# Kernel optimization log

Hardware: AMD Instinct MI355X
Metric: run time of the kernel (lower is better)

## Reference

```python
import jax, jax.numpy as jnp
import numpy as np

B, T, D, KQ, K, V, L = 4, 4096, 256, 32, 4, 8, 4
LN_EPS = 1e-5


def _layernorm(h, g, b):
    mu = h.mean(-1, keepdims=True)
    var = ((h - mu) ** 2).mean(-1, keepdims=True)
    return (h - mu) * jax.lax.rsqrt(var + LN_EPS) * g + b


def _forward(x, attention_mask, Wq, bq, Wk, bk, Wg, bg, W1f, b1f, W2f, b2f,
             ln_g, ln_b, Whh, b_ih, b_hh, Wp, bp, opW1, opb1, opW2, opb2, Wo, bo):
    # ---- DemandRouter ----
    q = x @ Wq + bq                      # [B,T,KQ]
    k = x @ Wk + bk                      # [B,T,KQ]
    sim = jnp.einsum('btk,bsk->bts', q, k) / jnp.sqrt(jnp.float32(KQ))  # [B,T,T]
    mask2 = attention_mask[:, None, :] * attention_mask[:, :, None]
    sim = jnp.where(mask2 == 0, jnp.float32(-1e9), sim)
    gates = jax.nn.sigmoid(x @ Wg + bg)[..., 0]   # [B,T]
    sim = sim * gates[:, :, None]
    _, idx = jax.lax.top_k(sim, K)                # [B,T,K]
    gathered = jax.vmap(lambda xb, ib: xb[ib])(x, idx)  # [B,T,K,D]
    routed_mean = gathered.mean(axis=2)           # [B,T,D]
    # ---- System1Block ----
    ffn = jax.nn.gelu(routed_mean @ W1f + b1f, approximate=False) @ W2f + b2f
    h = _layernorm(routed_mean + ffn, ln_g, ln_b)  # [B,T,D]
    # ---- ProgramGenerator (GRU over zero inputs, h0 = mean-pooled context) ----
    hs = h.mean(axis=1)                           # [B,D]
    outs = []
    for _ in range(L):
        gh = hs @ Whh.T + b_hh                    # [B,3D]
        r = jax.nn.sigmoid(b_ih[:D] + gh[:, :D])
        z = jax.nn.sigmoid(b_ih[D:2 * D] + gh[:, D:2 * D])
        n = jnp.tanh(b_ih[2 * D:] + r * gh[:, 2 * D:])
        hs = (1 - z) * n + z * hs
        outs.append(hs)
    rnn_out = jnp.stack(outs, axis=1)             # [B,L,D]
    program_logits = rnn_out @ Wp + bp            # [B,L,V]
    # ---- NeuralOpLibrary: op outputs are identical across L, so compute once
    # on [B,T,D] and average softmax weights over L (same math as expand+mean).
    op_hidden = jax.nn.relu(jnp.einsum('btd,vde->btve', h, opW1) + opb1)
    op_out = jnp.einsum('btve,ved->btvd', op_hidden, opW2) + opb2  # [B,T,V,D]
    w = jax.nn.softmax(program_logits, axis=-1).mean(axis=1)       # [B,V]
    fused = jnp.einsum('bv,btvd->btd', w, op_out)                   # [B,T,D]
    # ---- pool + output projection ----
    pooled = fused.max(axis=1)                    # [B,D]
    return pooled @ Wo + bo


def setup_inputs() -> dict:
    key = jax.random.key(0)
    ks = jax.random.split(key, 20)
    s = 0.02
    p = lambda i, shape: jax.random.normal(ks[i], shape, jnp.float32) * s
    return {
        'x': jax.random.normal(ks[0], (B, T, D), jnp.float32),
        'attention_mask': jnp.ones((B, T), jnp.float32),
        'Wq': p(1, (D, KQ)), 'bq': jnp.zeros((KQ,), jnp.float32),
        'Wk': p(2, (D, KQ)), 'bk': jnp.zeros((KQ,), jnp.float32),
        'Wg': p(3, (D, 1)), 'bg': jnp.zeros((1,), jnp.float32),
        'W1f': p(4, (D, 2 * D)), 'b1f': jnp.zeros((2 * D,), jnp.float32),
        'W2f': p(5, (2 * D, D)), 'b2f': jnp.zeros((D,), jnp.float32),
        'ln_g': jnp.ones((D,), jnp.float32), 'ln_b': jnp.zeros((D,), jnp.float32),
        'Whh': p(6, (3 * D, D)), 'b_ih': p(7, (3 * D,)), 'b_hh': p(8, (3 * D,)),
        'Wp': p(9, (D, V)), 'bp': jnp.zeros((V,), jnp.float32),
        'opW1': p(10, (V, D, D)), 'opb1': jnp.zeros((V, D), jnp.float32),
        'opW2': p(11, (V, D, D)), 'opb2': jnp.zeros((V, D), jnp.float32),
        'Wo': p(12, (D, D)), 'bo': jnp.zeros((D,), jnp.float32),
    }


def reference(x, attention_mask, Wq, bq, Wk, bk, Wg, bg, W1f, b1f, W2f, b2f,
              ln_g, ln_b, Whh, b_ih, b_hh, Wp, bp, opW1, opb1, opW2, opb2, Wo, bo):
    return _forward(x, attention_mask, Wq, bq, Wk, bk, Wg, bg, W1f, b1f, W2f, b2f,
                    ln_g, ln_b, Whh, b_ih, b_hh, Wp, bp, opW1, opb1, opW2, opb2, Wo, bo)
```

## Files before the change

### kernel.cpp

```cpp
#include <hip/hip_runtime.h>

#define BB 4
#define TT 4096
#define DD 256
#define KQ 32
#define TOPK 4
#define NV 8
#define NL 4
#define MROWS (BB*TT)
#define NSC 8
#define SSPAN 512
#define NCAND (NSC*16)

typedef __attribute__((ext_vector_type(8))) __bf16 bf16x8;
typedef __attribute__((ext_vector_type(4))) float  f32x4;

__device__ __forceinline__ unsigned short f2bf(float f) {
  union { float f; unsigned u; } un; un.f = f;
  unsigned r = un.u + 0x7fffu + ((un.u >> 16) & 1u);
  return (unsigned short)(r >> 16);
}
__device__ __forceinline__ float b2f(unsigned short s) {
  union { unsigned u; float f; } un; un.u = ((unsigned)s) << 16;
  return un.f;
}

__device__ __forceinline__ void ins4(float val, int s, float v[4], int id[4]) {
  if (val <= v[3]) return;
  v[3] = val; id[3] = s;
  #pragma unroll
  for (int j = 3; j > 0; --j) {
    if (v[j] > v[j-1]) {
      float tv = v[j]; v[j] = v[j-1]; v[j-1] = tv;
      int   ti = id[j]; id[j] = id[j-1]; id[j-1] = ti;
    }
  }
}

__global__ __launch_bounds__(256) void prep_weights(
    const float* __restrict__ W1f, const float* __restrict__ W2f,
    const float* __restrict__ opW1, const float* __restrict__ opW2,
    const float* __restrict__ Whh,
    unsigned short* __restrict__ W1ft, unsigned short* __restrict__ W2ft,
    unsigned short* __restrict__ opW1t, unsigned short* __restrict__ opW2t,
    unsigned int* __restrict__ Whhp) {
  int idx = blockIdx.x * 256 + threadIdx.x;
  if (idx < 131072) { int n = idx >> 8, d = idx & 255; W1ft[idx] = f2bf(W1f[d*512 + n]); return; }
  idx -= 131072;
  if (idx < 131072) { int n = idx >> 9, d = idx & 511; W2ft[idx] = f2bf(W2f[d*256 + n]); return; }
  idx -= 131072;
  if (idx < 524288) { int np = idx >> 8, d = idx & 255; int v = np >> 8, e = np & 255;
                      opW1t[idx] = f2bf(opW1[v*65536 + d*256 + e]); return; }
  idx -= 524288;
  if (idx < 524288) { int n = idx >> 11, kp = idx & 2047; int v = kp >> 8, k2 = kp & 255;
                      opW2t[idx] = f2bf(opW2[v*65536 + k2*256 + n]); return; }
  idx -= 524288;
  if (idx < 98304) {
    int dp = idx / 768, j = idx - dp*768;
    unsigned lo = f2bf(Whh[j*256 + 2*dp]);
    unsigned hi = f2bf(Whh[j*256 + 2*dp + 1]);
    Whhp[idx] = lo | (hi << 16);
  }
}

__global__ __launch_bounds__(256) void qk_proj(
    const float* __restrict__ x, const float* __restrict__ Wq, const float* __restrict__ bq,
    const float* __restrict__ Wk, const float* __restrict__ bk,
    float* __restrict__ q, float* __restrict__ kk,
    unsigned short* __restrict__ qbf, unsigned short* __restrict__ kbf) {
  __shared__ float xs[1024];
  int tid = threadIdx.x;
  *(float4*)&xs[tid*4] = *(const float4*)&x[(size_t)blockIdx.x*1024 + tid*4];
  __syncthreads();
  int row = blockIdx.x*4 + (tid >> 6);
  int j = tid & 63;
  int jj = j & 31;
  const float* W = (j < 32) ? Wq : Wk;
  const float* xr = &xs[(tid >> 6) * 256];
  float acc = 0.f;
  #pragma unroll 8
  for (int d = 0; d < 256; ++d) acc += xr[d] * W[d*32 + jj];
  acc += (j < 32) ? bq[jj] : bk[jj];
  float* out = (j < 32) ? q : kk;
  unsigned short* outb = (j < 32) ? qbf : kbf;
  out[(size_t)row*32 + jj] = acc;
  outb[(size_t)row*32 + jj] = f2bf(acc);
}

__global__ __launch_bounds__(256) void sim_scan(
    const unsigned short* __restrict__ qbf, const unsigned short* __restrict__ kbf,
    const float* __restrict__ mask, int* __restrict__ candi, float* __restrict__ candvv) {
  int b = blockIdx.z, sc = blockIdx.y;
  int q0 = blockIdx.x * 64;
  int tid = threadIdx.x;
  int w = tid >> 6, lane = tid & 63;
  int l15 = lane & 15, lhi = lane >> 4;

  __shared__ unsigned short kfr[SSPAN*32];
  __shared__ float ms[SSPAN];
  __shared__ int mflag;

  int qrow = q0 + w*16 + l15;
  bf16x8 qf = *(const bf16x8*)&qbf[((size_t)b*TT + qrow)*32 + lhi*8];
  float mrow = mask[b*TT + qrow];

  float vtop[4]; int itop[4];
  #pragma unroll
  for (int r = 0; r < 4; ++r) { vtop[r] = -__builtin_inff(); itop[r] = 0; }

  int s0 = sc * SSPAN;
  if (tid == 0) mflag = 0;
  __syncthreads();
  int anyzero = 0;
  #pragma unroll
  for (int rr = 0; rr < 2; ++rr) {
    int s = rr*256 + tid;
    const unsigned short* src = &kbf[((size_t)b*TT + s0 + s)*32];
    uint4 d0 = *(const uint4*)(src);
    uint4 d1 = *(const uint4*)(src + 8);
    uint4 d2 = *(const uint4*)(src + 16);
    uint4 d3 = *(const uint4*)(src + 24);
    int fb = (s >> 4)*512 + (s & 15)*8;
    *(uint4*)&kfr[fb +   0] = d0;
    *(uint4*)&kfr[fb + 128] = d1;
    *(uint4*)&kfr[fb + 256] = d2;
    *(uint4*)&kfr[fb + 384] = d3;
    float mv = mask[b*TT + s0 + s];
    ms[s] = mv;
    if (mv == 0.f) anyzero = 1;
  }
  if (anyzero) mflag = 1;
  __syncthreads();
  bool useMask = (mflag != 0) || (mrow == 0.f);
  f32x4 z = {0.f, 0.f, 0.f, 0.f};
  for (int sf = 0; sf < SSPAN/16; sf += 2) {
    bf16x8 a0 = *(const bf16x8*)&kfr[(sf+0)*512 + lane*8];
    bf16x8 a1 = *(const bf16x8*)&kfr[(sf+1)*512 + lane*8];
    f32x4 c0 = __builtin_amdgcn_mfma_f32_16x16x32_bf16(a0, qf, z, 0, 0, 0);
    f32x4 c1 = __builtin_amdgcn_mfma_f32_16x16x32_bf16(a1, qf, z, 0, 0, 0);
    int sb0 = s0 + (sf+0)*16 + lhi*4;
    int sb1 = s0 + (sf+1)*16 + lhi*4;
    #pragma unroll
    for (int r = 0; r < 4; ++r) {
      float v0 = c0[r], v1 = c1[r];
      if (useMask) {
        if (mrow * ms[(sf+0)*16 + lhi*4 + r] == 0.f) v0 = -1e9f;
        if (mrow * ms[(sf+1)*16 + lhi*4 + r] == 0.f) v1 = -1e9f;
      }
      ins4(v0, sb0 + r, vtop, itop);
      ins4(v1, sb1 + r, vtop, itop);
    }
  }
  size_t base = ((size_t)(b*TT + qrow))*NCAND + sc*16 + lhi*4;
  #pragma unroll
  for (int r = 0; r < 4; ++r) { candi[base + r] = itop[r]; candvv[base + r] = vtop[r]; }
}

__global__ __launch_bounds__(256) void refine8(
    const int* __restrict__ candi, const float* __restrict__ candv,
    const float* __restrict__ q, const float* __restrict__ kk,
    const float* __restrict__ mask, int* __restrict__ sel) {
  int tid = threadIdx.x;
  int g = tid >> 5, j = tid & 31;
  int row = blockIdx.x*8 + g;
  int b = row >> 12;
  float v[4]; int id[4];
  const float* cvp = &candv[(size_t)row*NCAND];
  const int*   cip = &candi[(size_t)row*NCAND];
  #pragma unroll
  for (int k2 = 0; k2 < 4; ++k2) { v[k2] = cvp[j + k2*32]; id[k2] = cip[j + k2*32]; }
  int c8[8];
  #pragma unroll
  for (int r = 0; r < 8; ++r) {
    float bv = v[0]; int bi = id[0];
    #pragma unroll
    for (int k2 = 1; k2 < 4; ++k2)
      if (v[k2] > bv || (v[k2] == bv && id[k2] < bi)) { bv = v[k2]; bi = id[k2]; }
    #pragma unroll
    for (int o = 16; o > 0; o >>= 1) {
      float ov = __shfl_xor(bv, o, 32);
      int   oi = __shfl_xor(bi, o, 32);
      if (ov > bv || (ov == bv && oi < bi)) { bv = ov; bi = oi; }
    }
    c8[r] = bi;
    #pragma unroll
    for (int k2 = 0; k2 < 4; ++k2) if (id[k2] == bi) v[k2] = -__builtin_inff();
  }
  int ca = c8[j >> 2];
  int seg = (j & 3) * 8;
  const float* kp = &kk[((size_t)(b << 12) + ca)*32 + seg];
  const float* qp = &q[(size_t)row*32 + seg];
  float pd = 0.f;
  #pragma unroll
  for (int t = 0; t < 8; t += 4) {
    float4 kv = *(const float4*)&kp[t];
    float4 qv = *(const float4*)&qp[t];
    pd += kv.x*qv.x + kv.y*qv.y + kv.z*qv.z + kv.w*qv.w;
  }
  pd += __shfl_xor(pd, 1, 32);
  pd += __shfl_xor(pd, 2, 32);
  if (mask[row] * mask[(b << 12) + ca] == 0.f) pd = -1e9f;
  float dv[8];
  #pragma unroll
  for (int c = 0; c < 8; ++c) dv[c] = __shfl(pd, c*4, 32);
  if (j == 0) {
    int s0 = -1, s1 = -1, s2 = -1, s3 = -1;
    int4 o4;
    #pragma unroll
    for (int r = 0; r < 4; ++r) {
      float bv = -__builtin_inff(); int bi = 0x7fffffff;
      #pragma unroll
      for (int c = 0; c < 8; ++c) {
        int ii = c8[c]; float vv = dv[c];
        if (ii == s0 || ii == s1 || ii == s2 || ii == s3) continue;
        if (vv > bv || (vv == bv && ii < bi)) { bv = vv; bi = ii; }
      }
      if (r == 0) { o4.x = bi; s0 = bi; }
      else if (r == 1) { o4.y = bi; s1 = bi; }
      else if (r == 2) { o4.z = bi; s2 = bi; }
      else { o4.w = bi; s3 = bi; }
    }
    *(int4*)&sel[(size_t)row*4] = o4;
  }
}

__global__ __launch_bounds__(256) void gather_mean(
    const int* __restrict__ sel, const float* __restrict__ x,
    unsigned short* __restrict__ rmb) {
  int tid = threadIdx.x;
  int row = blockIdx.x*4 + (tid >> 6);
  int lane = tid & 63;
  int b = row >> 12;
  int4 s = *(const int4*)&sel[(size_t)row*4];
  const float* xb = &x[(size_t)b*TT*DD];
  float4 a  = *(const float4*)&xb[(size_t)s.x*DD + lane*4];
  float4 bb = *(const float4*)&xb[(size_t)s.y*DD + lane*4];
  float4 cc = *(const float4*)&xb[(size_t)s.z*DD + lane*4];
  float4 e  = *(const float4*)&xb[(size_t)s.w*DD + lane*4];
  ushort4 o;
  o.x = f2bf((a.x + bb.x + cc.x + e.x)*0.25f);
  o.y = f2bf((a.y + bb.y + cc.y + e.y)*0.25f);
  o.z = f2bf((a.z + bb.z + cc.z + e.z)*0.25f);
  o.w = f2bf((a.w + bb.w + cc.w + e.w)*0.25f);
  *(ushort4*)&rmb[(size_t)row*DD + lane*4] = o;
}

template<int EPI>
__global__ __launch_bounds__(256) void gemm_bf16(
    const unsigned short* __restrict__ A, const unsigned short* __restrict__ Bt,
    int Ndim, int Kdim,
    const float* __restrict__ bias,
    const unsigned short* __restrict__ resB,
    const float* __restrict__ auxf,
    float* __restrict__ outF, unsigned short* __restrict__ outB) {
  __shared__ unsigned short SMEM[128*132];
  unsigned short* As = SMEM;
  unsigned short* Bs = SMEM + 128*64;
  int tid = threadIdx.x;
  int lane = tid & 63, wid = tid >> 6;
  int wm = wid >> 1, wn = wid & 1;
  int l16 = lane & 15, lhi = lane >> 4;
  int m0 = blockIdx.x * 128, n0 = blockIdx.y * 128;
  f32x4 acc[4][4] = {};
  for (int kt = 0; kt < Kdim; kt += 64) {
    __syncthreads();
    #pragma unroll
    for (int i = 0; i < 4; ++i) {
      int L = i*256 + tid;
      int r = L >> 3, c = L & 7;
      int cs = c ^ (r & 7);
      uint4 va = *(const uint4*)(A  + (size_t)(m0 + r)*Kdim + kt + c*8);
      *(uint4*)&As[r*64 + cs*8] = va;
      uint4 vb = *(const uint4*)(Bt + (size_t)(n0 + r)*Kdim + kt + c*8);
      *(uint4*)&Bs[r*64 + cs*8] = vb;
    }
    __syncthreads();
    #pragma unroll
    for (int ks = 0; ks < 2; ++ks) {
      bf16x8 af[4], bfr[4];
      int kc = ks*4 + lhi;
      #pragma unroll
      for (int f = 0; f < 4; ++f) {
        int ra = wm*64 + f*16 + l16;
        af[f]  = *(const bf16x8*)&As[ra*64 + ((kc ^ (ra & 7)))*8];
        int rb = wn*64 + f*16 + l16;
        bfr[f] = *(const bf16x8*)&Bs[rb*64 + ((kc ^ (rb & 7)))*8];
      }
      #pragma unroll
      for (int mf = 0; mf < 4; ++mf)
        #pragma unroll
        for (int nf = 0; nf < 4; ++nf)
          acc[mf][nf] = __builtin_amdgcn_mfma_f32_16x16x32_bf16(af[mf], bfr[nf], acc[mf][nf], 0, 0, 0);
    }
  }
  if constexpr (EPI == 1) {
    #pragma unroll
    for (int mf = 0; mf < 4; ++mf)
      #pragma unroll
      for (int nf = 0; nf < 4; ++nf)
        #pragma unroll
        for (int r = 0; r < 4; ++r) {
          int row = m0 + wm*64 + mf*16 + lhi*4 + r;
          int col = n0 + wn*64 + nf*16 + l16;
          float v = acc[mf][nf][r] + bias[col] + b2f(resB[(size_t)row*Ndim + col]);
          outF[(size_t)row*Ndim + col] = v;
        }
  } else {
    __syncthreads();
    #pragma unroll
    for (int mf = 0; mf < 4; ++mf) {
      #pragma unroll
      for (int nf = 0; nf < 4; ++nf) {
        #pragma unroll
        for (int r = 0; r < 4; ++r) {
          int lrow = wm*64 + mf*16 + lhi*4 + r;
          int lcol = wn*64 + nf*16 + l16;
          int row = m0 + lrow, col = n0 + lcol;
          float v = acc[mf][nf][r];
          if constexpr (EPI == 0) {
            v += bias[col];
            v = 0.5f * v * (1.0f + erff(v * 0.70710678118654752f));
          } else if constexpr (EPI == 2) {
            v += bias[col];
            v = fmaxf(v, 0.0f) * auxf[(row >> 12)*8 + (col >> 8)];
          } else {
            v += auxf[(row >> 12)*256 + col];
          }
          SMEM[lrow*132 + lcol] = f2bf(v);
        }
      }
    }
    __syncthreads();
    #pragma unroll
    for (int i = 0; i < 8; ++i) {
      int idx = i*256 + tid;
      int lrow = idx >> 4, co = (idx & 15)*8;
      *(uint4*)&outB[(size_t)(m0 + lrow)*Ndim + n0 + co] = *(const uint4*)&SMEM[lrow*132 + co];
    }
  }
}

__global__ __launch_bounds__(256) void gemm64_bf16(
    const unsigned short* __restrict__ A, const unsigned short* __restrict__ Bt,
    int Ndim, int Kdim,
    const float* __restrict__ auxf, unsigned short* __restrict__ outB) {
  __shared__ unsigned short SMEM[64*192 + 64];
  unsigned short* As = SMEM;
  unsigned short* Bs = SMEM + 64*64;
  int tid = threadIdx.x;
  int lane = tid & 63, wn = tid >> 6;
  int l16 = lane & 15, lhi = lane >> 4;
  int m0 = blockIdx.x * 64, n0 = blockIdx.y * 128;
  f32x4 acc[4][2] = {};
  for (int kt = 0; kt < Kdim; kt += 64) {
    __syncthreads();
    #pragma unroll
    for (int i = 0; i < 2; ++i) {
      int L = i*256 + tid;
      int r = L >> 3, c = L & 7;
      int cs = c ^ (r & 7);
      uint4 va = *(const uint4*)(A + (size_t)(m0 + r)*Kdim + kt + c*8);
      *(uint4*)&As[r*64 + cs*8] = va;
    }
    #pragma unroll
    for (int i = 0; i < 4; ++i) {
      int L = i*256 + tid;
      int r = L >> 3, c = L & 7;
      int cs = c ^ (r & 7);
      uint4 vb = *(const uint4*)(Bt + (size_t)(n0 + r)*Kdim + kt + c*8);
      *(uint4*)&Bs[r*64 + cs*8] = vb;
    }
    __syncthreads();
    #pragma unroll
    for (int ks = 0; ks < 2; ++ks) {
      bf16x8 af[4], bfr[2];
      int kc = ks*4 + lhi;
      #pragma unroll
      for (int f = 0; f < 4; ++f) {
        int ra = f*16 + l16;
        af[f] = *(const bf16x8*)&As[ra*64 + ((kc ^ (ra & 7)))*8];
      }
      #pragma unroll
      for (int f = 0; f < 2; ++f) {
        int rb = wn*32 + f*16 + l16;
        bfr[f] = *(const bf16x8*)&Bs[rb*64 + ((kc ^ (rb & 7)))*8];
      }
      #pragma unroll
      for (int mf = 0; mf < 4; ++mf)
        #pragma unroll
        for (int nf = 0; nf < 2; ++nf)
          acc[mf][nf] = __builtin_amdgcn_mfma_f32_16x16x32_bf16(af[mf], bfr[nf], acc[mf][nf], 0, 0, 0);
    }
  }
  __syncthreads();
  #pragma unroll
  for (int mf = 0; mf < 4; ++mf) {
    #pragma unroll
    for (int nf = 0; nf < 2; ++nf) {
      #pragma unroll
      for (int r = 0; r < 4; ++r) {
        int lrow = mf*16 + lhi*4 + r;
        int lcol = wn*32 + nf*16 + l16;
        float v = acc[mf][nf][r] + auxf[((m0 + lrow) >> 12)*256 + n0 + lcol];
        SMEM[lrow*132 + lcol] = f2bf(v);
      }
    }
  }
  __syncthreads();
  #pragma unroll
  for (int i = 0; i < 4; ++i) {
    int idx = i*256 + tid;
    int lrow = idx >> 4, co = (idx & 15)*8;
    *(uint4*)&outB[(size_t)(m0 + lrow)*Ndim + n0 + co] = *(const uint4*)&SMEM[lrow*132 + co];
  }
}

__global__ __launch_bounds__(256) void ln_kernel(
    const float* __restrict__ preLN, const float* __restrict__ g,
    const float* __restrict__ bta, unsigned short* __restrict__ h) {
  int tid = threadIdx.x;
  int lane = tid & 63;
  int row = blockIdx.x*4 + (tid >> 6);
  float4 v = *(const float4*)&preLN[(size_t)row*256 + lane*4];
  float s = v.x + v.y + v.z + v.w;
  #pragma unroll
  for (int o = 32; o > 0; o >>= 1) s += __shfl_xor(s, o);
  float mu = s * (1.0f/256.0f);
  float4 d; d.x = v.x-mu; d.y = v.y-mu; d.z = v.z-mu; d.w = v.w-mu;
  float s2 = d.x*d.x + d.y*d.y + d.z*d.z + d.w*d.w;
  #pragma unroll
  for (int o = 32; o > 0; o >>= 1) s2 += __shfl_xor(s2, o);
  float rstd = rsqrtf(s2 * (1.0f/256.0f) + 1e-5f);
  float4 gv = *(const float4*)&g[lane*4];
  float4 bv = *(const float4*)&bta[lane*4];
  ushort4 o;
  o.x = f2bf(d.x*rstd*gv.x + bv.x);
  o.y = f2bf(d.y*rstd*gv.y + bv.y);
  o.z = f2bf(d.z*rstd*gv.z + bv.z);
  o.w = f2bf(d.w*rstd*gv.w + bv.w);
  *(ushort4*)&h[(size_t)row*256 + lane*4] = o;
}

__global__ __launch_bounds__(256) void hsum_kernel(const unsigned short* __restrict__ h, float* __restrict__ hpart) {
  int c = blockIdx.x, b = blockIdx.y, d = threadIdx.x;
  const unsigned short* hp = &h[((size_t)(b*TT + c*64))*256 + d];
  float s = 0.f;
  #pragma unroll 8
  for (int i = 0; i < 64; ++i) s += b2f(hp[i*256]);
  hpart[(b*64 + c)*256 + d] = s;
}

__global__ __launch_bounds__(1024) void gru_kernel(
    const float* __restrict__ hpart, const unsigned int* __restrict__ Whhp,
    const float* __restrict__ b_ih, const float* __restrict__ b_hh,
    const float* __restrict__ Wp, const float* __restrict__ bp,
    const float* __restrict__ opb2, float* __restrict__ w, float* __restrict__ wb2) {
  int b = blockIdx.x, tid = threadIdx.x;
  __shared__ float hs[256];
  __shared__ float gsh[768];
  __shared__ float wps[2048];
  __shared__ float lgpart[256];
  __shared__ float lg[8];
  __shared__ float wacc[8];
  if (tid < 256) {
    float s = 0.f;
    #pragma unroll
    for (int c = 0; c < 64; ++c) s += hpart[(b*64 + c)*256 + tid];
    hs[tid] = s * (1.0f/4096.0f);
  }
  wps[tid] = Wp[tid];
  wps[1024 + tid] = Wp[1024 + tid];
  if (tid < 8) wacc[tid] = 0.f;
  __syncthreads();
  for (int l = 0; l < NL; ++l) {
    if (tid < 768) {
      float acc = 0.f;
      #pragma unroll 16
      for (int dp = 0; dp < 128; ++dp) {
        unsigned w2 = Whhp[dp*768 + tid];
        acc += b2f((unsigned short)(w2 & 0xffff))*hs[2*dp]
             + b2f((unsigned short)(w2 >> 16))*hs[2*dp + 1];
      }
      gsh[tid] = acc;
    }
    __syncthreads();
    if (tid < 256) {
      float g0 = gsh[tid]       + b_hh[tid];
      float g1 = gsh[256 + tid] + b_hh[256 + tid];
      float g2 = gsh[512 + tid] + b_hh[512 + tid];
      float r = 1.f / (1.f + expf(-(b_ih[tid] + g0)));
      float z = 1.f / (1.f + expf(-(b_ih[256 + tid] + g1)));
      float n = tanhf(b_ih[512 + tid] + r * g2);
      gsh[tid] = (1.f - z) * n + z * hs[tid];
    }
    __syncthreads();
    if (tid < 256) hs[tid] = gsh[tid];
    __syncthreads();
    if (tid < 256) {
      int dp2 = tid >> 3;
      float acc = 0.f;
      #pragma unroll
      for (int k2 = 0; k2 < 8; ++k2) acc += hs[dp2 + 32*k2] * wps[tid + 256*k2];
      lgpart[tid] = acc;
    }
    __syncthreads();
    if (tid < 8) {
      float acc = bp[tid];
      #pragma unroll
      for (int j = 0; j < 32; ++j) acc += lgpart[j*8 + tid];
      lg[tid] = acc;
    }
    __syncthreads();
    if (tid == 0) {
      float mx = lg[0];
      #pragma unroll
      for (int i = 1; i < 8; ++i) mx = fmaxf(mx, lg[i]);
      float sm = 0.f; float e[8];
      #pragma unroll
      for (int i = 0; i < 8; ++i) { e[i] = expf(lg[i] - mx); sm += e[i]; }
      #pragma unroll
      for (int i = 0; i < 8; ++i) wacc[i] += e[i] / sm;
    }
    __syncthreads();
  }
  if (tid < 8) w[b*8 + tid] = wacc[tid] * 0.25f;
  if (tid < 256) {
    float acc = 0.f;
    #pragma unroll
    for (int v = 0; v < 8; ++v) acc += (wacc[v] * 0.25f) * opb2[v*256 + tid];
    wb2[b*256 + tid] = acc;
  }
}

__global__ __launch_bounds__(256) void maxpool_kernel(const unsigned short* __restrict__ fusedB, float* __restrict__ mpart) {
  int c = blockIdx.x, b = blockIdx.y, d = threadIdx.x;
  const unsigned short* fp = &fusedB[((size_t)(b*TT + c*64))*256 + d];
  float m = -__builtin_inff();
  #pragma unroll 8
  for (int i = 0; i < 64; ++i) m = fmaxf(m, b2f(fp[i*256]));
  mpart[(b*64 + c)*256 + d] = m;
}

__global__ __launch_bounds__(256) void outproj_kernel(
    const float* __restrict__ mpart, const float* __restrict__ Wo,
    const float* __restrict__ bo, float* __restrict__ out) {
  int b = blockIdx.x, tid = threadIdx.x;
  __shared__ float pooled[256];
  float m = -__builtin_inff();
  for (int c = 0; c < 64; ++c) m = fmaxf(m, mpart[(b*64 + c)*256 + tid]);
  pooled[tid] = m;
  __syncthreads();
  float acc = bo[tid];
  for (int d = 0; d < 256; ++d) acc += pooled[d] * Wo[d*256 + tid];
  out[b*256 + tid] = acc;
}

extern "C" void kernel_launch(void* const* d_in, const int* in_sizes, int n_in,
                              void* d_out, int out_size, void* d_ws, size_t ws_size,
                              hipStream_t stream) {
  const float* x     = (const float*)d_in[0];
  const float* amask = (const float*)d_in[1];
  const float* Wq    = (const float*)d_in[2];
  const float* bq    = (const float*)d_in[3];
  const float* Wk    = (const float*)d_in[4];
  const float* bk    = (const float*)d_in[5];
  const float* W1f   = (const float*)d_in[8];
  const float* b1f   = (const float*)d_in[9];
  const float* W2f   = (const float*)d_in[10];
  const float* b2f   = (const float*)d_in[11];
  const float* ln_g  = (const float*)d_in[12];
  const float* ln_b  = (const float*)d_in[13];
  const float* Whh   = (const float*)d_in[14];
  const float* b_ih  = (const float*)d_in[15];
  const float* b_hh  = (const float*)d_in[16];
  const float* Wp    = (const float*)d_in[17];
  const float* bp    = (const float*)d_in[18];
  const float* opW1  = (const float*)d_in[19];
  const float* opb1  = (const float*)d_in[20];
  const float* opW2  = (const float*)d_in[21];
  const float* opb2  = (const float*)d_in[22];
  const float* Wo    = (const float*)d_in[23];
  const float* bo    = (const float*)d_in[24];
  (void)in_sizes; (void)n_in; (void)out_size; (void)ws_size;

  char* ws = (char*)d_ws;
  float*          q      = (float*)(ws + 0);
  float*          kk     = (float*)(ws + 2097152);
  unsigned short* qbf    = (unsigned short*)(ws + 4194304);
  unsigned short* kbf    = (unsigned short*)(ws + 5242880);
  int*            candi  = (int*)(ws + 6291456);
  float*          candv  = (float*)(ws + 14680064);
  unsigned short* rmb    = (unsigned short*)(ws + 23068672);
  unsigned short* G1     = (unsigned short*)(ws + 31457280);
  float*          preLN  = (float*)(ws + 48234496);
  unsigned short* G1all  = (unsigned short*)(ws + 0);
  unsigned short* h      = (unsigned short*)(ws + 67108864);
  unsigned short* W1ft   = (unsigned short*)(ws + 75497472);
  unsigned short* W2ft   = (unsigned short*)(ws + 75759616);
  unsigned short* opW1t  = (unsigned short*)(ws + 76021760);
  unsigned short* opW2t  = (unsigned short*)(ws + 77070336);
  unsigned int*   Whhp   = (unsigned int*)(ws + 78118912);
  float*          hpart  = (float*)(ws + 78512128);
  float*          wv     = (float*)(ws + 78774272);
  float*          wb2    = (float*)(ws + 78778368);
  float*          mpart  = (float*)(ws + 78782464);
  unsigned short* fusedB = (unsigned short*)(ws + 79044608);
  int*            sel    = (int*)(ws + 87433216);

  prep_weights<<<5504, 256, 0, stream>>>(W1f, W2f, opW1, opW2, Whh, W1ft, W2ft, opW1t, opW2t, Whhp);
  qk_proj<<<4096, 256, 0, stream>>>(x, Wq, bq, Wk, bk, q, kk, qbf, kbf);
  sim_scan<<<dim3(TT/64, NSC, BB), 256, 0, stream>>>(qbf, kbf, amask, candi, candv);
  refine8<<<MROWS/8, 256, 0, stream>>>(candi, candv, q, kk, amask, sel);
  gather_mean<<<MROWS/4, 256, 0, stream>>>(sel, x, rmb);
  gemm_bf16<0><<<dim3(128, 4), 256, 0, stream>>>(rmb, W1ft, 512, 256, b1f, nullptr, nullptr, nullptr, G1);
  gemm_bf16<1><<<dim3(128, 2), 256, 0, stream>>>(G1, W2ft, 256, 512, b2f, rmb, nullptr, preLN, nullptr);
  ln_kernel<<<4096, 256, 0, stream>>>(preLN, ln_g, ln_b, h);
  hsum_kernel<<<dim3(64, BB), 256, 0, stream>>>(h, hpart);
  gru_kernel<<<4, 1024, 0, stream>>>(hpart, Whhp, b_ih, b_hh, Wp, bp, opb2, wv, wb2);
  gemm_bf16<2><<<dim3(128, 16), 256, 0, stream>>>(h, opW1t, 2048, 256, opb1, nullptr, wv, nullptr, G1all);
  gemm64_bf16<<<dim3(256, 2), 256, 0, stream>>>(G1all, opW2t, 256, 2048, wb2, fusedB);
  maxpool_kernel<<<dim3(64, BB), 256, 0, stream>>>(fusedB, mpart);
  outproj_kernel<<<4, 256, 0, stream>>>(mpart, Wo, bo, (float*)d_out);
}
```

Measured before the change: 291.7 us.

## Fuse FFN up-projection, GELU, down-projection, residual and LayerNorm into one kernel

```diff
diff --git a/kernel.cpp b/kernel.cpp
--- a/kernel.cpp
+++ b/kernel.cpp
@@ -245,6 +245,123 @@
   *(ushort4*)&rmb[(size_t)row*DD + lane*4] = o;
 }
 
+__global__ __launch_bounds__(512) void ffn_fused(
+    const unsigned short* __restrict__ rmb,
+    const unsigned short* __restrict__ W1ft,
+    const unsigned short* __restrict__ W2ft,
+    const float* __restrict__ b1f, const float* __restrict__ bias2,
+    const float* __restrict__ ln_g, const float* __restrict__ ln_b,
+    unsigned short* __restrict__ h) {
+  __shared__ unsigned short rmbS[64*264];
+  __shared__ unsigned short G1S[64*520];
+  __shared__ float psum[64][8];
+  __shared__ float psq[64][8];
+  __shared__ float meanS[64];
+  __shared__ float rstdS[64];
+  int tid = threadIdx.x;
+  int w = tid >> 6, lane = tid & 63, l16 = lane & 15, lhi = lane >> 4;
+  int m0 = blockIdx.x * 64;
+  #pragma unroll
+  for (int i = 0; i < 4; ++i) {
+    int idx = i*512 + tid;
+    int r = idx >> 5, c = (idx & 31) * 8;
+    *(uint4*)&rmbS[r*264 + c] = *(const uint4*)&rmb[(size_t)(m0 + r)*256 + c];
+  }
+  __syncthreads();
+  {
+    f32x4 acc1[4][4] = {};
+    #pragma unroll
+    for (int kk2 = 0; kk2 < 8; ++kk2) {
+      int ko = kk2*32 + lhi*8;
+      bf16x8 af[4], bf[4];
+      #pragma unroll
+      for (int f = 0; f < 4; ++f) af[f] = *(const bf16x8*)&rmbS[(f*16 + l16)*264 + ko];
+      #pragma unroll
+      for (int f = 0; f < 4; ++f) bf[f] = *(const bf16x8*)&W1ft[(size_t)(w*64 + f*16 + l16)*256 + ko];
+      #pragma unroll
+      for (int mf = 0; mf < 4; ++mf)
+        #pragma unroll
+        for (int nf = 0; nf < 4; ++nf)
+          acc1[mf][nf] = __builtin_amdgcn_mfma_f32_16x16x32_bf16(af[mf], bf[nf], acc1[mf][nf], 0, 0, 0);
+    }
+    #pragma unroll
+    for (int mf = 0; mf < 4; ++mf) {
+      #pragma unroll
+      for (int nf = 0; nf < 4; ++nf) {
+        int col = w*64 + nf*16 + l16;
+        float bias = b1f[col];
+        #pragma unroll
+        for (int r = 0; r < 4; ++r) {
+          int row = mf*16 + lhi*4 + r;
+          float v = acc1[mf][nf][r] + bias;
+          v = 0.5f * v * (1.0f + erff(v * 0.70710678118654752f));
+          G1S[row*520 + col] = f2bf(v);
+        }
+      }
+    }
+  }
+  __syncthreads();
+  f32x4 acc2[4][2] = {};
+  #pragma unroll
+  for (int kk2 = 0; kk2 < 16; ++kk2) {
+    int ko = kk2*32 + lhi*8;
+    bf16x8 af[4], bf[2];
+    #pragma unroll
+    for (int f = 0; f < 4; ++f) af[f] = *(const bf16x8*)&G1S[(f*16 + l16)*520 + ko];
+    #pragma unroll
+    for (int f = 0; f < 2; ++f) bf[f] = *(const bf16x8*)&W2ft[(size_t)(w*32 + f*16 + l16)*512 + ko];
+    #pragma unroll
+    for (int mf = 0; mf < 4; ++mf)
+      #pragma unroll
+      for (int nf = 0; nf < 2; ++nf)
+        acc2[mf][nf] = __builtin_amdgcn_mfma_f32_16x16x32_bf16(af[mf], bf[nf], acc2[mf][nf], 0, 0, 0);
+  }
+  float pre[4][2][4];
+  #pragma unroll
+  for (int mf = 0; mf < 4; ++mf) {
+    #pragma unroll
+    for (int r = 0; r < 4; ++r) {
+      int row = mf*16 + lhi*4 + r;
+      float s = 0.f, sq = 0.f;
+      #pragma unroll
+      for (int nf = 0; nf < 2; ++nf) {
+        int col = w*32 + nf*16 + l16;
+        float v = acc2[mf][nf][r] + bias2[col] + b2f(rmbS[row*264 + col]);
+        pre[mf][nf][r] = v;
+        s += v; sq += v*v;
+      }
+      #pragma unroll
+      for (int o = 1; o < 16; o <<= 1) { s += __shfl_xor(s, o); sq += __shfl_xor(sq, o); }
+      if (l16 == 0) { psum[row][w] = s; psq[row][w] = sq; }
+    }
+  }
+  __syncthreads();
+  if (tid < 64) {
+    float s = 0.f, sq = 0.f;
+    #pragma unroll
+    for (int j = 0; j < 8; ++j) { s += psum[tid][j]; sq += psq[tid][j]; }
+    float mean = s * (1.0f/256.0f);
+    float var = sq * (1.0f/256.0f) - mean*mean;
+    meanS[tid] = mean;
+    rstdS[tid] = rsqrtf(var + 1e-5f);
+  }
+  __syncthreads();
+  #pragma unroll
+  for (int nf = 0; nf < 2; ++nf) {
+    int col = w*32 + nf*16 + l16;
+    float gv = ln_g[col], bv = ln_b[col];
+    #pragma unroll
+    for (int mf = 0; mf < 4; ++mf) {
+      #pragma unroll
+      for (int r = 0; r < 4; ++r) {
+        int row = mf*16 + lhi*4 + r;
+        float v = (pre[mf][nf][r] - meanS[row]) * rstdS[row] * gv + bv;
+        h[(size_t)(m0 + row)*256 + col] = f2bf(v);
+      }
+    }
+  }
+}
+
 template<int EPI>
 __global__ __launch_bounds__(256) void gemm_bf16(
     const unsigned short* __restrict__ A, const unsigned short* __restrict__ Bt,
@@ -415,32 +532,6 @@
   }
 }
 
-__global__ __launch_bounds__(256) void ln_kernel(
-    const float* __restrict__ preLN, const float* __restrict__ g,
-    const float* __restrict__ bta, unsigned short* __restrict__ h) {
-  int tid = threadIdx.x;
-  int lane = tid & 63;
-  int row = blockIdx.x*4 + (tid >> 6);
-  float4 v = *(const float4*)&preLN[(size_t)row*256 + lane*4];
-  float s = v.x + v.y + v.z + v.w;
-  #pragma unroll
-  for (int o = 32; o > 0; o >>= 1) s += __shfl_xor(s, o);
-  float mu = s * (1.0f/256.0f);
-  float4 d; d.x = v.x-mu; d.y = v.y-mu; d.z = v.z-mu; d.w = v.w-mu;
-  float s2 = d.x*d.x + d.y*d.y + d.z*d.z + d.w*d.w;
-  #pragma unroll
-  for (int o = 32; o > 0; o >>= 1) s2 += __shfl_xor(s2, o);
-  float rstd = rsqrtf(s2 * (1.0f/256.0f) + 1e-5f);
-  float4 gv = *(const float4*)&g[lane*4];
-  float4 bv = *(const float4*)&bta[lane*4];
-  ushort4 o;
-  o.x = f2bf(d.x*rstd*gv.x + bv.x);
-  o.y = f2bf(d.y*rstd*gv.y + bv.y);
-  o.z = f2bf(d.z*rstd*gv.z + bv.z);
-  o.w = f2bf(d.w*rstd*gv.w + bv.w);
-  *(ushort4*)&h[(size_t)row*256 + lane*4] = o;
-}
-
 __global__ __launch_bounds__(256) void hsum_kernel(const unsigned short* __restrict__ h, float* __restrict__ hpart) {
   int c = blockIdx.x, b = blockIdx.y, d = threadIdx.x;
   const unsigned short* hp = &h[((size_t)(b*TT + c*64))*256 + d];
@@ -567,7 +658,7 @@
   const float* W1f   = (const float*)d_in[8];
   const float* b1f   = (const float*)d_in[9];
   const float* W2f   = (const float*)d_in[10];
-  const float* b2f   = (const float*)d_in[11];
+  const float* b2fp  = (const float*)d_in[11];
   const float* ln_g  = (const float*)d_in[12];
   const float* ln_b  = (const float*)d_in[13];
   const float* Whh   = (const float*)d_in[14];
@@ -591,8 +682,6 @@
   int*            candi  = (int*)(ws + 6291456);
   float*          candv  = (float*)(ws + 14680064);
   unsigned short* rmb    = (unsigned short*)(ws + 23068672);
-  unsigned short* G1     = (unsigned short*)(ws + 31457280);
-  float*          preLN  = (float*)(ws + 48234496);
   unsigned short* G1all  = (unsigned short*)(ws + 0);
   unsigned short* h      = (unsigned short*)(ws + 67108864);
   unsigned short* W1ft   = (unsigned short*)(ws + 75497472);
@@ -612,9 +701,7 @@
   sim_scan<<<dim3(TT/64, NSC, BB), 256, 0, stream>>>(qbf, kbf, amask, candi, candv);
   refine8<<<MROWS/8, 256, 0, stream>>>(candi, candv, q, kk, amask, sel);
   gather_mean<<<MROWS/4, 256, 0, stream>>>(sel, x, rmb);
-  gemm_bf16<0><<<dim3(128, 4), 256, 0, stream>>>(rmb, W1ft, 512, 256, b1f, nullptr, nullptr, nullptr, G1);
-  gemm_bf16<1><<<dim3(128, 2), 256, 0, stream>>>(G1, W2ft, 256, 512, b2f, rmb, nullptr, preLN, nullptr);
-  ln_kernel<<<4096, 256, 0, stream>>>(preLN, ln_g, ln_b, h);
+  ffn_fused<<<MROWS/64, 512, 0, stream>>>(rmb, W1ft, W2ft, b1f, b2fp, ln_g, ln_b, h);
   hsum_kernel<<<dim3(64, BB), 256, 0, stream>>>(h, hpart);
   gru_kernel<<<4, 1024, 0, stream>>>(hpart, Whhp, b_ih, b_hh, Wp, bp, opb2, wv, wb2);
   gemm_bf16<2><<<dim3(128, 16), 256, 0, stream>>>(h, opW1t, 2048, 256, opb1, nullptr, wv, nullptr, G1all);
```

Measured after the change: 288.1 us. No clear change (-1.2%).
